# Performance work log

Measured on AMD Instinct MI355X. Metric: run time of the kernel, lower is better.

The kernel has to match this reference:

```python
import jax, jax.numpy as jnp
import numpy as np

D, H, T, P1, P2, B = 1024, 16, 2048, 16, 16, 2
HD = D // H
EPS = 1e-6
NEG = -1e30


def _ln(x, g, b):
    mu = jnp.mean(x, axis=-1, keepdims=True)
    var = jnp.mean((x - mu) ** 2, axis=-1, keepdims=True)
    return (x - mu) * jax.lax.rsqrt(var + EPS) * g + b


def _split_heads(x):  # [B,S,D] -> [B,H,S,HD]
    b, s, _ = x.shape
    return x.reshape(b, s, H, HD).transpose(0, 2, 1, 3)


def _merge_heads(x):  # [B,H,S,HD] -> [B,S,D]
    b, _, s, _ = x.shape
    return x.transpose(0, 2, 1, 3).reshape(b, s, D)


def setup_inputs() -> dict:
    key = jax.random.key(0)
    ks = jax.random.split(key, 24)
    s = 0.02
    inp = {
        'x': jax.random.normal(ks[0], (B, T, D), jnp.float32),
        'p1': jax.random.normal(ks[1], (B, P1, D), jnp.float32),
        'p2': jax.random.normal(ks[2], (B, P2, D), jnp.float32),
        'prior_1': jax.random.uniform(ks[3], (B, T), jnp.float32),
        'prior_2': jax.random.uniform(ks[4], (B, T), jnp.float32),
        'mask': jnp.ones((B, T), jnp.float32),
        'Wq': s * jax.random.normal(ks[5], (D, D), jnp.float32),
        'bq': jnp.zeros((D,), jnp.float32),
        'Wk': s * jax.random.normal(ks[6], (D, D), jnp.float32),
        'bk': jnp.zeros((D,), jnp.float32),
        'Wv': s * jax.random.normal(ks[7], (D, D), jnp.float32),
        'bv': jnp.zeros((D,), jnp.float32),
        'ln2_g': jnp.ones((D,), jnp.float32),
        'ln2_b': jnp.zeros((D,), jnp.float32),
        'W1': s * jax.random.normal(ks[8], (D, D), jnp.float32),
        'b1': jnp.zeros((D,), jnp.float32),
        'W2': s * jax.random.normal(ks[9], (D, D), jnp.float32),
        'b2': jnp.zeros((D,), jnp.float32),
        'Wp1': s * jax.random.normal(ks[10], (D, D), jnp.float32),
        'bp1': jnp.zeros((D,), jnp.float32),
        'Wp2': s * jax.random.normal(ks[11], (D, D), jnp.float32),
        'bp2': jnp.zeros((D,), jnp.float32),
    }
    return inp


def reference(x, p1, p2, prior_1, prior_2, mask, Wq, bq, Wk, bk, Wv, bv,
              ln2_g, ln2_b, W1, b1, W2, b2, Wp1, bp1, Wp2, bp2):
    scale = 1.0 / jnp.sqrt(jnp.asarray(HD, x.dtype))
    # Q/K are [proj(x); p1; p2] (prompts enter unprojected), V only from x.
    q = _split_heads(jnp.concatenate([x @ Wq + bq, p1, p2], axis=1))
    k = _split_heads(jnp.concatenate([x @ Wk + bk, p1, p2], axis=1))
    v = _split_heads(x @ Wv + bv)
    scores = jnp.einsum('bhqd,bhkd->bhqk', q, k) * scale  # [B,H,T+P,T+P]

    word = scores[:, :, :T, :T]                                  # [B,H,T,T]
    p1s = jnp.swapaxes(scores[:, :, :T, T:T + P1], -1, -2)       # [B,H,P1,T]
    p2s = jnp.swapaxes(scores[:, :, :T, T + P1:], -1, -2)        # [B,H,P2,T]

    word = word + (1.0 - mask)[:, None, None, :] * NEG           # mask_logits
    wa = jax.nn.softmax(word, axis=-1)
    p1a = jax.nn.softmax(jax.nn.softmax(p1s, axis=-1) * prior_1[:, None, None, :], axis=-1)
    p2a = jax.nn.softmax(jax.nn.softmax(p2s, axis=-1) * prior_2[:, None, None, :], axis=-1)

    ctx = jnp.einsum('bhqk,bhkd->bhqd', wa, v)    # [B,H,T,HD]
    p1_v = jnp.einsum('bhpk,bhkd->bhpd', p1a, ctx)
    p2_v = jnp.einsum('bhpk,bhkd->bhpd', p2a, ctx)

    residual = x + _merge_heads(ctx)
    out = _ln(residual, ln2_g, ln2_b)
    out = jax.nn.gelu(out @ W1 + b1, approximate=False)
    out = out @ W2 + b2 + residual

    p1_out = _ln(_merge_heads(p1_v) + p1, ln2_g, ln2_b)
    p1_out = jax.nn.gelu(p1_out @ Wp1 + bp1, approximate=False)

    p2_out = _ln(_merge_heads(p2_v) + p2, ln2_g, ln2_b)
    p2_out = jax.nn.gelu(p2_out @ Wp2 + bp2, approximate=False)
    return (out, p1_out, p2_out)
```

## Files before the change

kernel.cpp:

```cpp
#include <hip/hip_runtime.h>

#define DEV __device__ __forceinline__

typedef unsigned short u16;
typedef unsigned int   u32;
typedef short  s16x8  __attribute__((ext_vector_type(8)));
typedef float  f32x4  __attribute__((ext_vector_type(4)));
typedef float  f32x16 __attribute__((ext_vector_type(16)));

constexpr int Bc = 2, Hc = 16, Tc = 2048, Dc = 1024, HDc = 64, Mc = 4096;
constexpr int TP = Tc + 32;
constexpr float SCALEc = 0.125f;
constexpr float LOG2E = 1.44269504088896340736f;
constexpr float SCALE2c = SCALEc * LOG2E;
constexpr float NEGc = -1e30f;

typedef __attribute__((address_space(3))) void lds_void;
typedef const __attribute__((address_space(1))) void g_void;

DEV void gload16(const void* g, void* l) {
  __builtin_amdgcn_global_load_lds((g_void*)g, (lds_void*)l, 16, 0, 0);
}

DEV int swz(int r) { return (r & 7) ^ ((r >> 3) & 7); }

DEV u32 bfr(float f) {
  u32 u = __float_as_uint(f);
  return (u + 0x7fffu + ((u >> 16) & 1u)) >> 16;
}
DEV u32 cvtpk(float a, float b) {
  u32 r;
  asm("v_cvt_pk_bf16_f32 %0, %1, %2" : "=v"(r) : "v"(a), "v"(b));
  return r;
}
DEV s16x8 mk8(u32 w0, u32 w1, u32 w2, u32 w3) {
  union { u32 u[4]; s16x8 v; } x;
  x.u[0] = w0; x.u[1] = w1; x.u[2] = w2; x.u[3] = w3;
  return x.v;
}
DEV float geluf(float x) { return 0.5f * x * (1.0f + erff(x * 0.70710678118654752440f)); }

DEV float wredS(float v) {
  #pragma unroll
  for (int o = 32; o; o >>= 1) v += __shfl_xor(v, o);
  return v;
}
DEV float wredM(float v) {
  #pragma unroll
  for (int o = 32; o; o >>= 1) v = fmaxf(v, __shfl_xor(v, o));
  return v;
}
DEV float bredS(float v, float* sm) {
  v = wredS(v);
  __syncthreads();
  if ((threadIdx.x & 63) == 0) sm[threadIdx.x >> 6] = v;
  __syncthreads();
  return sm[0] + sm[1] + sm[2] + sm[3];
}
DEV float bredM(float v, float* sm) {
  v = wredM(v);
  __syncthreads();
  if ((threadIdx.x & 63) == 0) sm[threadIdx.x >> 6] = v;
  __syncthreads();
  return fmaxf(fmaxf(sm[0], sm[1]), fmaxf(sm[2], sm[3]));
}

__global__ __launch_bounds__(256) void transpose_w_k(const float* __restrict__ src,
                                                     u16* __restrict__ dst) {
  __shared__ float tile[32][33];
  int bx = blockIdx.x, by = blockIdx.y;
  int tx = threadIdx.x & 31, ty = threadIdx.x >> 5;
  #pragma unroll
  for (int i = 0; i < 32; i += 8)
    tile[ty + i][tx] = src[(size_t)(by * 32 + ty + i) * Dc + bx * 32 + tx];
  __syncthreads();
  #pragma unroll
  for (int i = 0; i < 32; i += 8)
    dst[(size_t)(bx * 32 + ty + i) * Dc + by * 32 + tx] = (u16)bfr(tile[tx][ty + i]);
}

__global__ __launch_bounds__(256) void cvt_bf16_k(const float* __restrict__ in,
                                                  u16* __restrict__ out, int n4) {
  int i = blockIdx.x * 256 + threadIdx.x;
  if (i < n4) {
    float4 v = ((const float4*)in)[i];
    ushort4 u;
    u.x = (u16)bfr(v.x); u.y = (u16)bfr(v.y); u.z = (u16)bfr(v.z); u.w = (u16)bfr(v.w);
    ((ushort4*)out)[i] = u;
  }
}

__global__ __launch_bounds__(256) void kprompt_k(const float* __restrict__ p1,
                                                 const float* __restrict__ p2,
                                                 u16* __restrict__ kb) {
  int i = blockIdx.x * 256 + threadIdx.x;
  int d = i & 63, j = (i >> 6) & 31, h = (i >> 11) & 15, b = i >> 15;
  float v = (j < 16) ? p1[(size_t)(b * 16 + j) * Dc + h * 64 + d]
                     : p2[(size_t)(b * 16 + j - 16) * Dc + h * 64 + d];
  kb[(((size_t)(b * Hc + h) * TP + Tc + j) << 6) + d] = (u16)bfr(v);
}

__global__ __launch_bounds__(256) void vtrans_k(const u16* __restrict__ vb,
                                                u16* __restrict__ vt) {
  __shared__ u16 tl[64][65];
  int bh = blockIdx.x >> 5, tc = blockIdx.x & 31;
  int d = threadIdx.x & 63, r = threadIdx.x >> 6;
  #pragma unroll
  for (int i = 0; i < 64; i += 4)
    tl[r + i][d] = vb[(((size_t)bh * Tc + tc * 64 + r + i) << 6) + d];
  __syncthreads();
  int t = threadIdx.x & 63, dd = threadIdx.x >> 6;
  #pragma unroll
  for (int i = 0; i < 64; i += 4)
    vt[((size_t)bh * 64 + dd + i) * Tc + tc * 64 + t] = tl[t][dd + i];
}

template <int MODE, int NBX>
__global__ __launch_bounds__(256, 3) void gemm128_k(
    const u16* __restrict__ A, const u16* __restrict__ Bt,
    const float* __restrict__ bias0, const float* __restrict__ bias1,
    const float* __restrict__ bias2,
    u16* __restrict__ outQ, u16* __restrict__ outK, u16* __restrict__ outV,
    u16* __restrict__ outB, float* __restrict__ outF,
    const float* __restrict__ resid) {
  __shared__ __align__(16) u16 smem[17408];
  u16* as0 = smem;
  u16* bs0 = smem + 2 * 128 * 32;
  const int tid = threadIdx.x, lane = tid & 63, wave = tid >> 6;
  const int wr = wave >> 1, wc = wave & 1;
  const int nwg = gridDim.x, bid = (int)blockIdx.x;
  const int wg = (bid & 7) * (nwg >> 3) + (bid >> 3);
  const int row0 = (wg % NBX) * 128, col0 = (wg / NBX) * 128;

  f32x4 zero4;
  #pragma unroll
  for (int r = 0; r < 4; ++r) zero4[r] = 0.f;
  f32x4 acc[4][4];
  #pragma unroll
  for (int i = 0; i < 4; ++i)
    #pragma unroll
    for (int j = 0; j < 4; ++j) acc[i][j] = zero4;

  auto stage = [&](int buf, int kt) {
    const int k0 = kt * 32;
    #pragma unroll
    for (int is = 0; is < 2; ++is) {
      int q = is * 256 + tid; int r = q >> 2, c = q & 3, g = c ^ ((r >> 1) & 3);
      gload16(A + (size_t)(row0 + r) * Dc + k0 + g * 8,
              as0 + (size_t)buf * 4096 + (is * 256 + wave * 64) * 8);
    }
    #pragma unroll
    for (int is = 0; is < 2; ++is) {
      int q = is * 256 + tid; int r = q >> 2, c = q & 3, g = c ^ ((r >> 1) & 3);
      gload16(Bt + (size_t)(col0 + r) * Dc + k0 + g * 8,
              bs0 + (size_t)buf * 4096 + (is * 256 + wave * 64) * 8);
    }
  };

  stage(0, 0);
  asm volatile("s_waitcnt vmcnt(0)" ::: "memory");
  __syncthreads();

  int cur = 0;
  for (int kt = 0; kt < 32; ++kt) {
    if (kt + 1 < 32) stage(cur ^ 1, kt + 1);
    s16x8 af[4], bfv[4];
    #pragma unroll
    for (int f = 0; f < 4; ++f) {
      int r = wr * 64 + f * 16 + (lane & 15);
      int c = (lane >> 4) ^ ((r >> 1) & 3);
      af[f] = *(const s16x8*)&as0[cur * 4096 + r * 32 + c * 8];
    }
    #pragma unroll
    for (int f = 0; f < 4; ++f) {
      int r = wc * 64 + f * 16 + (lane & 15);
      int c = (lane >> 4) ^ ((r >> 1) & 3);
      bfv[f] = *(const s16x8*)&bs0[cur * 4096 + r * 32 + c * 8];
    }
    __builtin_amdgcn_s_setprio(1);
    #pragma unroll
    for (int i = 0; i < 4; ++i)
      #pragma unroll
      for (int j = 0; j < 4; ++j)
        acc[i][j] = __builtin_amdgcn_mfma_f32_16x16x32_bf16(af[i], bfv[j], acc[i][j], 0, 0, 0);
    __builtin_amdgcn_s_setprio(0);
    __syncthreads();
    cur ^= 1;
  }

  if (MODE == 0 || MODE == 1) {
    const int CS = 136;
    u16* ct = smem;
    #pragma unroll
    for (int i = 0; i < 4; ++i)
      #pragma unroll
      for (int j = 0; j < 4; ++j)
        #pragma unroll
        for (int r = 0; r < 4; ++r) {
          int rl = wr * 64 + i * 16 + (lane >> 4) * 4 + r;
          int cl = wc * 64 + j * 16 + (lane & 15);
          float v = acc[i][j][r];
          if (MODE == 0) {
            int n = (col0 + cl) & 1023;
            int which = (col0 + cl) >> 10;
            v += (which == 0 ? bias0 : (which == 1 ? bias1 : bias2))[n];
          } else {
            v = geluf(v + bias0[col0 + cl]);
          }
          ct[rl * CS + cl] = (u16)bfr(v);
        }
    __syncthreads();
    #pragma unroll
    for (int it = 0; it < 16; ++it) {
      int linear = it * 256 + tid;
      int row = linear >> 5, c4 = (linear & 31) * 4;
      ushort4 val = *(const ushort4*)&ct[row * CS + c4];
      int grow = row0 + row;
      if (MODE == 1) {
        *(ushort4*)&outB[(size_t)grow * Dc + col0 + c4] = val;
      } else {
        int col = col0 + c4;
        int which = col >> 10, n = col & 1023;
        int hh = n >> 6, d = n & 63, bb = grow >> 11, t = grow & 2047;
        if (which == 0)
          *(ushort4*)&outQ[(((size_t)(bb * Hc + hh) * Tc + t) << 6) + d] = val;
        else if (which == 1)
          *(ushort4*)&outK[(((size_t)(bb * Hc + hh) * TP + t) << 6) + d] = val;
        else
          *(ushort4*)&outV[(((size_t)(bb * Hc + hh) * Tc + t) << 6) + d] = val;
      }
    }
  } else {
    const int CSF = 132;
    float* cf = (float*)smem;
    #pragma unroll
    for (int p = 0; p < 2; ++p) {
      if (wr == p) {
        #pragma unroll
        for (int i = 0; i < 4; ++i)
          #pragma unroll
          for (int j = 0; j < 4; ++j)
            #pragma unroll
            for (int r = 0; r < 4; ++r) {
              int rl = i * 16 + (lane >> 4) * 4 + r;
              int cl = wc * 64 + j * 16 + (lane & 15);
              cf[rl * CSF + cl] = acc[i][j][r];
            }
      }
      __syncthreads();
      #pragma unroll
      for (int it = 0; it < 8; ++it) {
        int linear = it * 256 + tid;
        int row = linear >> 5, c4 = (linear & 31) * 4;
        float4 v = *(const float4*)&cf[row * CSF + c4];
        int grow = row0 + p * 64 + row;
        int col = col0 + c4;
        float4 rr = *(const float4*)&resid[(size_t)grow * Dc + col];
        float4 o;
        o.x = v.x + bias0[col + 0] + rr.x;
        o.y = v.y + bias0[col + 1] + rr.y;
        o.z = v.z + bias0[col + 2] + rr.z;
        o.w = v.w + bias0[col + 3] + rr.w;
        *(float4*)&outF[(size_t)grow * Dc + col] = o;
      }
      __syncthreads();
    }
  }
}

__global__ __launch_bounds__(256, 2) void attn_k(
    const u16* __restrict__ qb,
    const u16* __restrict__ kb,
    const u16* __restrict__ vt,
    const float* __restrict__ maskp,
    float* __restrict__ OP0, float* __restrict__ OP1,
    float* __restrict__ ML) {
  __shared__ __align__(16) u16 kls[2][64 * 64];
  __shared__ __align__(16) u16 vls[2][64 * 64];
  __shared__ float mls[1024];

  const int tid = threadIdx.x, lane = tid & 63, wave = tid >> 6;
  const int wg = ((int)blockIdx.x & 7) * 128 + ((int)blockIdx.x >> 3);
  const int ks = wg & 1, qt = (wg >> 1) & 15, bh = wg >> 5;
  const int b = bh >> 4;
  const int lo = lane & 31, h5 = lane >> 5;
  const size_t kbase = (size_t)bh * TP * 64;
  const size_t vbase = (size_t)bh * 64 * Tc;

  for (int i = tid; i < 1024; i += 256)
    mls[i] = (1.0f - maskp[(size_t)b * Tc + ks * 1024 + i]) * NEGc;

  const int q0 = qt * 128 + wave * 32;
  s16x8 qf[4];
  #pragma unroll
  for (int kc = 0; kc < 4; ++kc)
    qf[kc] = *(const s16x8*)(qb + ((size_t)bh * Tc + q0 + lo) * 64 + kc * 16 + h5 * 8);

  auto stageKV = [&](int buf, int kt2) {
    #pragma unroll
    for (int is = 0; is < 2; ++is) {
      int q = is * 256 + tid; int r = q >> 3, c = q & 7, g = c ^ swz(r);
      gload16(kb + kbase + (size_t)(kt2 * 64 + r) * 64 + g * 8,
              &kls[buf][(is * 256 + wave * 64) * 8]);
      gload16(vt + vbase + (size_t)r * Tc + kt2 * 64 + g * 8,
              &vls[buf][(is * 256 + wave * 64) * 8]);
    }
  };

  stageKV(0, ks * 16);
  asm volatile("s_waitcnt vmcnt(0)" ::: "memory");
  __syncthreads();

  f32x16 zero16;
  #pragma unroll
  for (int r = 0; r < 16; ++r) zero16[r] = 0.f;
  f32x16 O0 = zero16, O1 = zero16, racc = zero16;

  int cur = 0;
  for (int kt = 0; kt < 16; ++kt) {
    if (kt + 1 < 16) stageKV(cur ^ 1, ks * 16 + kt + 1);

    #pragma unroll
    for (int c = 0; c < 2; ++c) {
      f32x16 s = zero16;
      __builtin_amdgcn_s_setprio(1);
      #pragma unroll
      for (int kc = 0; kc < 4; ++kc) {
        int r = c * 32 + lo;
        int ci = (kc * 2 + h5) ^ swz(r);
        s16x8 kf = *(const s16x8*)&kls[cur][r * 64 + ci * 8];
        s = __builtin_amdgcn_mfma_f32_32x32x16_bf16(kf, qf[kc], s, 0, 0, 0);
      }
      __builtin_amdgcn_s_setprio(0);

      float4 mq[4];
      #pragma unroll
      for (int g = 0; g < 4; ++g)
        mq[g] = *(const float4*)&mls[kt * 64 + c * 32 + 4 * h5 + 8 * g];

      float p[16];
      #pragma unroll
      for (int r = 0; r < 16; ++r) {
        float mv = (&mq[r >> 2].x)[r & 3];
        p[r] = exp2f(s[r] * SCALE2c + mv);
        racc[r] += p[r];
      }

      #pragma unroll
      for (int k1 = 0; k1 < 2; ++k1) {
        u32 w0 = cvtpk(p[8 * k1 + 0], p[8 * k1 + 1]);
        u32 w1 = cvtpk(p[8 * k1 + 2], p[8 * k1 + 3]);
        u32 w2 = cvtpk(p[8 * k1 + 4], p[8 * k1 + 5]);
        u32 w3 = cvtpk(p[8 * k1 + 6], p[8 * k1 + 7]);
        asm volatile("v_permlane32_swap_b32 %0, %1" : "+v"(w2), "+v"(w0));
        asm volatile("v_permlane32_swap_b32 %0, %1" : "+v"(w3), "+v"(w1));
        s16x8 pf = mk8(w0, w1, w2, w3);
        __builtin_amdgcn_s_setprio(1);
        #pragma unroll
        for (int db = 0; db < 2; ++db) {
          int d = db * 32 + lo;
          int ci = (c * 4 + k1 * 2 + h5) ^ swz(d);
          s16x8 vf = *(const s16x8*)&vls[cur][d * 64 + ci * 8];
          if (db == 0) O0 = __builtin_amdgcn_mfma_f32_32x32x16_bf16(pf, vf, O0, 0, 0, 0);
          else         O1 = __builtin_amdgcn_mfma_f32_32x32x16_bf16(pf, vf, O1, 0, 0, 0);
        }
        __builtin_amdgcn_s_setprio(0);
      }
    }
    __syncthreads();
    cur ^= 1;
  }

  float* dst = ks ? OP1 : OP0;
  #pragma unroll
  for (int r = 0; r < 16; ++r) {
    int row = q0 + (r & 3) + 8 * (r >> 2) + 4 * h5;
    dst[((size_t)bh * Tc + row) * 64 + lo]      = O0[r];
    dst[((size_t)bh * Tc + row) * 64 + 32 + lo] = O1[r];
  }
  float lt = 0.f;
  #pragma unroll
  for (int r = 0; r < 16; ++r) lt += racc[r];
  lt += __shfl_xor(lt, 32);
  if (lane < 32)
    ML[((size_t)ks * 32 + bh) * Tc + q0 + lo] = lt;
}

__global__ __launch_bounds__(256) void combine_k(const float* __restrict__ OP0,
                                                 const float* __restrict__ OP1,
                                                 const float* __restrict__ ML,
                                                 float* __restrict__ ctx) {
  int idx = blockIdx.x * 256 + threadIdx.x;
  int row = idx >> 4;
  int c4 = (idx & 15) * 4;
  float linv = 1.0f / (ML[(size_t)row] + ML[(size_t)32 * Tc + row]);
  float4 v0 = *(const float4*)(OP0 + (size_t)row * 64 + c4);
  float4 v1 = *(const float4*)(OP1 + (size_t)row * 64 + c4);
  float4 o;
  o.x = (v0.x + v1.x) * linv;
  o.y = (v0.y + v1.y) * linv;
  o.z = (v0.z + v1.z) * linv;
  o.w = (v0.w + v1.w) * linv;
  *(float4*)(ctx + (size_t)row * 64 + c4) = o;
}

__global__ __launch_bounds__(256) void promptsc_k(const u16* __restrict__ qb,
                                                  const u16* __restrict__ kb,
                                                  float* __restrict__ SP) {
  __shared__ __align__(16) u16 kpls[32 * 64];
  const int tid = threadIdx.x, lane = tid & 63, wave = tid >> 6;
  const int qt = blockIdx.x, bh = blockIdx.y;
  const int lo = lane & 31, h5 = lane >> 5;
  const size_t kbase = (size_t)bh * TP * 64;

  {
    int r = tid >> 3, c = tid & 7, g = c ^ swz(r);
    gload16(kb + kbase + (size_t)(Tc + r) * 64 + g * 8, &kpls[wave * 64 * 8]);
  }
  const int q0 = qt * 128 + wave * 32;
  s16x8 qf[4];
  #pragma unroll
  for (int kc = 0; kc < 4; ++kc)
    qf[kc] = *(const s16x8*)(qb + ((size_t)bh * Tc + q0 + lo) * 64 + kc * 16 + h5 * 8);
  asm volatile("s_waitcnt vmcnt(0)" ::: "memory");
  __syncthreads();

  f32x16 sp;
  #pragma unroll
  for (int r = 0; r < 16; ++r) sp[r] = 0.f;
  #pragma unroll
  for (int kc = 0; kc < 4; ++kc) {
    int ci = (kc * 2 + h5) ^ swz(lo);
    s16x8 kf = *(const s16x8*)&kpls[lo * 64 + ci * 8];
    sp = __builtin_amdgcn_mfma_f32_32x32x16_bf16(kf, qf[kc], sp, 0, 0, 0);
  }
  #pragma unroll
  for (int r = 0; r < 16; ++r) {
    int pr = (r & 3) + 8 * (r >> 2) + 4 * h5;
    SP[((size_t)bh * 32 + pr) * Tc + q0 + lo] = sp[r] * SCALEc;
  }
}

__global__ __launch_bounds__(256) void prompt_softmax_k(float* __restrict__ SP,
                                                        const float* __restrict__ pr1,
                                                        const float* __restrict__ pr2) {
  __shared__ float sm[4];
  int row = blockIdx.x;
  int bh = row >> 5, p = row & 31, b = bh >> 4;
  const float* prior = (p < 16 ? pr1 : pr2) + (size_t)b * Tc;
  float* s = SP + (size_t)row * Tc;
  int tid = threadIdx.x;
  float v[8], pw[8];
  #pragma unroll
  for (int i = 0; i < 8; ++i) { int t = tid + i * 256; v[i] = s[t]; pw[i] = prior[t]; }
  float mx = -INFINITY;
  #pragma unroll
  for (int i = 0; i < 8; ++i) mx = fmaxf(mx, v[i]);
  mx = bredM(mx, sm);
  float sum = 0.f;
  #pragma unroll
  for (int i = 0; i < 8; ++i) { v[i] = __expf(v[i] - mx); sum += v[i]; }
  sum = bredS(sum, sm);
  float inv = 1.0f / sum;
  float mx2 = -INFINITY;
  #pragma unroll
  for (int i = 0; i < 8; ++i) { v[i] = v[i] * inv * pw[i]; mx2 = fmaxf(mx2, v[i]); }
  mx2 = bredM(mx2, sm);
  float sum2 = 0.f;
  #pragma unroll
  for (int i = 0; i < 8; ++i) { v[i] = __expf(v[i] - mx2); sum2 += v[i]; }
  sum2 = bredS(sum2, sm);
  float inv2 = 1.0f / sum2;
  #pragma unroll
  for (int i = 0; i < 8; ++i) s[tid + i * 256] = v[i] * inv2;
}

__global__ __launch_bounds__(256) void pv_partial_k(const float* __restrict__ PA,
                                                    const float* __restrict__ ctx,
                                                    float* __restrict__ PVP) {
  __shared__ float pal[32][128];
  const int bh = blockIdx.x, ts = blockIdx.y;
  const int tid = threadIdx.x;
  const int t0 = ts * 128;
  const float* pabase = PA + (size_t)bh * 32 * Tc;

  #pragma unroll
  for (int i = 0; i < 4; ++i) {
    int e = tid + i * 256;
    int p = e >> 5, c4 = e & 31;
    *(float4*)&pal[p][c4 * 4] = *(const float4*)&pabase[(size_t)p * Tc + t0 + c4 * 4];
  }
  __syncthreads();

  const int d4 = tid & 15, p0 = tid >> 4;
  const float* cb = ctx + ((size_t)bh * Tc + t0) * 64 + d4 * 4;
  float4 a0 = make_float4(0.f, 0.f, 0.f, 0.f);
  float4 a1 = make_float4(0.f, 0.f, 0.f, 0.f);
  for (int tt = 0; tt < 128; ++tt) {
    float4 v = *(const float4*)(cb + (size_t)tt * 64);
    float w0 = pal[p0][tt], w1 = pal[p0 + 16][tt];
    a0.x += w0 * v.x; a0.y += w0 * v.y; a0.z += w0 * v.z; a0.w += w0 * v.w;
    a1.x += w1 * v.x; a1.y += w1 * v.y; a1.z += w1 * v.z; a1.w += w1 * v.w;
  }
  float* o = PVP + (((size_t)ts * 32 + bh) * 32) * 64 + d4 * 4;
  *(float4*)(o + (size_t)p0 * 64) = a0;
  *(float4*)(o + (size_t)(p0 + 16) * 64) = a1;
}

__global__ __launch_bounds__(256) void pv_reduce_k(const float* __restrict__ PVP,
                                                   float* __restrict__ PVo) {
  int e = blockIdx.x * 256 + threadIdx.x;
  float s = 0.f;
  #pragma unroll
  for (int ts = 0; ts < 16; ++ts) s += PVP[(size_t)ts * 65536 + e];
  PVo[e] = s;
}

__global__ __launch_bounds__(256) void resln_k(const float* __restrict__ x,
                                               const float* __restrict__ ctx,
                                               const float* __restrict__ g,
                                               const float* __restrict__ be,
                                               float* __restrict__ res,
                                               u16* __restrict__ lnout) {
  __shared__ float sm[4];
  int row = blockIdx.x;
  int b = row >> 11, t = row & 2047;
  int tid = threadIdx.x, c4 = tid * 4;
  int h = c4 >> 6, d = c4 & 63;
  float4 xv = *(const float4*)(x + (size_t)row * Dc + c4);
  float4 cv = *(const float4*)(ctx + (((size_t)(b * Hc + h) * Tc + t) << 6) + d);
  float r0 = xv.x + cv.x, r1 = xv.y + cv.y, r2 = xv.z + cv.z, r3 = xv.w + cv.w;
  float4 rr; rr.x = r0; rr.y = r1; rr.z = r2; rr.w = r3;
  *(float4*)(res + (size_t)row * Dc + c4) = rr;
  float s = bredS(r0 + r1 + r2 + r3, sm);
  float sq = bredS(r0 * r0 + r1 * r1 + r2 * r2 + r3 * r3, sm);
  float mu = s * (1.0f / Dc);
  float var = sq * (1.0f / Dc) - mu * mu;
  float rs = rsqrtf(var + 1e-6f);
  ushort4 o;
  o.x = (u16)bfr((r0 - mu) * rs * g[c4 + 0] + be[c4 + 0]);
  o.y = (u16)bfr((r1 - mu) * rs * g[c4 + 1] + be[c4 + 1]);
  o.z = (u16)bfr((r2 - mu) * rs * g[c4 + 2] + be[c4 + 2]);
  o.w = (u16)bfr((r3 - mu) * rs * g[c4 + 3] + be[c4 + 3]);
  *(ushort4*)(lnout + (size_t)row * Dc + c4) = o;
}

__global__ __launch_bounds__(256) void promptln_k(const float* __restrict__ PVo,
                                                  const float* __restrict__ p1,
                                                  const float* __restrict__ p2,
                                                  const float* __restrict__ g,
                                                  const float* __restrict__ be,
                                                  float* __restrict__ PMLN) {
  __shared__ float sm[4];
  int row = blockIdx.x;
  int b = row >> 5, j = row & 31;
  int tid = threadIdx.x, c4 = tid * 4;
  int h = c4 >> 6, d = c4 & 63;
  const float* pr = (j < 16) ? (p1 + (size_t)(b * 16 + j) * Dc + c4)
                             : (p2 + (size_t)(b * 16 + j - 16) * Dc + c4);
  float4 pv4 = *(const float4*)(PVo + (((size_t)(b * Hc + h) * 32 + j) << 6) + d);
  float4 pp4 = *(const float4*)pr;
  float r0 = pv4.x + pp4.x, r1 = pv4.y + pp4.y, r2 = pv4.z + pp4.z, r3 = pv4.w + pp4.w;
  float s = bredS(r0 + r1 + r2 + r3, sm);
  float sq = bredS(r0 * r0 + r1 * r1 + r2 * r2 + r3 * r3, sm);
  float mu = s * (1.0f / Dc);
  float var = sq * (1.0f / Dc) - mu * mu;
  float rs = rsqrtf(var + 1e-6f);
  float4 o;
  o.x = (r0 - mu) * rs * g[c4 + 0] + be[c4 + 0];
  o.y = (r1 - mu) * rs * g[c4 + 1] + be[c4 + 1];
  o.z = (r2 - mu) * rs * g[c4 + 2] + be[c4 + 2];
  o.w = (r3 - mu) * rs * g[c4 + 3] + be[c4 + 3];
  *(float4*)(PMLN + (size_t)row * Dc + c4) = o;
}

__global__ __launch_bounds__(256) void pffn_partial_k(const float* __restrict__ PMLN,
                                                      const float* __restrict__ Wp1,
                                                      const float* __restrict__ Wp2,
                                                      float* __restrict__ PB) {
  __shared__ float pm[32][32];
  const int tid = threadIdx.x;
  const int ks = blockIdx.x, ct = blockIdx.y, s = blockIdx.z;
  const int c = ct * 256 + tid;
  const int k0 = ks * 32;
  const float* W = s ? Wp2 : Wp1;

  #pragma unroll
  for (int i = 0; i < 4; ++i) {
    int e = tid + i * 256;
    int r = e >> 5, kk = e & 31;
    int grow = (r >> 4) * 32 + s * 16 + (r & 15);
    pm[r][kk] = PMLN[(size_t)grow * Dc + k0 + kk];
  }
  __syncthreads();

  float acc[32];
  #pragma unroll
  for (int r = 0; r < 32; ++r) acc[r] = 0.f;
  for (int kk = 0; kk < 32; ++kk) {
    float w = W[(size_t)(k0 + kk) * Dc + c];
    #pragma unroll
    for (int r = 0; r < 32; ++r) acc[r] += pm[r][kk] * w;
  }

  float* pb = PB + (((size_t)ks * 2 + s) * 32) * Dc + c;
  #pragma unroll
  for (int r = 0; r < 32; ++r) pb[(size_t)r * Dc] = acc[r];
}

__global__ __launch_bounds__(256) void pffn_reduce_k(const float* __restrict__ PB,
                                                     const float* __restrict__ bp1,
                                                     const float* __restrict__ bp2,
                                                     float* __restrict__ out) {
  int e = blockIdx.x * 256 + threadIdx.x;
  int s = e >> 15, rem = e & 32767;
  int r = rem >> 10, c = rem & 1023;
  float sum = 0.f;
  const float* pb = PB + ((size_t)s * 32 + r) * Dc + c;
  #pragma unroll
  for (int ks = 0; ks < 32; ++ks) sum += pb[(size_t)ks * 2 * 32 * Dc];
  const float* bp = s ? bp2 : bp1;
  out[(size_t)Mc * Dc + (size_t)s * (32 * Dc) + (size_t)r * Dc + c] = geluf(sum + bp[c]);
}

extern "C" void kernel_launch(void* const* d_in, const int* in_sizes, int n_in,
                              void* d_out, int out_size, void* d_ws, size_t ws_size,
                              hipStream_t stream) {
  (void)in_sizes; (void)n_in; (void)out_size; (void)ws_size;
  const float* x   = (const float*)d_in[0];
  const float* p1  = (const float*)d_in[1];
  const float* p2  = (const float*)d_in[2];
  const float* pr1 = (const float*)d_in[3];
  const float* pr2 = (const float*)d_in[4];
  const float* msk = (const float*)d_in[5];
  const float* Wq  = (const float*)d_in[6];
  const float* bq  = (const float*)d_in[7];
  const float* Wk  = (const float*)d_in[8];
  const float* bk  = (const float*)d_in[9];
  const float* Wv  = (const float*)d_in[10];
  const float* bv  = (const float*)d_in[11];
  const float* g2  = (const float*)d_in[12];
  const float* be2 = (const float*)d_in[13];
  const float* W1  = (const float*)d_in[14];
  const float* b1  = (const float*)d_in[15];
  const float* W2  = (const float*)d_in[16];
  const float* b2  = (const float*)d_in[17];
  const float* Wp1 = (const float*)d_in[18];
  const float* bp1 = (const float*)d_in[19];
  const float* Wp2 = (const float*)d_in[20];
  const float* bp2 = (const float*)d_in[21];

  char* ws = (char*)d_ws;
  size_t off = 0;
  auto alloc = [&](size_t bytes) {
    void* p = ws + off;
    off += (bytes + 255) & ~(size_t)255;
    return p;
  };
  u16* WQKVT = (u16*)alloc((size_t)3072 * 1024 * 2);
  u16* W1T   = (u16*)alloc((size_t)1024 * 1024 * 2);
  u16* W2T   = (u16*)alloc((size_t)1024 * 1024 * 2);
  u16* XB    = (u16*)alloc((size_t)Mc * Dc * 2);
  u16* QB    = (u16*)alloc((size_t)32 * Tc * 64 * 2);
  u16* KB    = (u16*)alloc((size_t)32 * TP * 64 * 2);
  u16* VB    = (u16*)alloc((size_t)32 * Tc * 64 * 2);
  u16* VT    = (u16*)alloc((size_t)32 * 64 * Tc * 2);
  float* CTX = (float*)alloc((size_t)32 * Tc * 64 * 4);
  float* SP  = (float*)alloc((size_t)32 * 32 * Tc * 4);
  float* PVo = (float*)alloc((size_t)32 * 32 * 64 * 4);
  float* RES = (float*)alloc((size_t)Mc * Dc * 4);
  float* PMLN = (float*)alloc((size_t)64 * Dc * 4);
  float* ML  = (float*)alloc((size_t)2 * 32 * Tc * 4);
  float* PVP = (float*)alloc((size_t)16 * 32 * 32 * 64 * 4);
  u16* LNOUT = XB;
  u16* H1    = VB;
  float* PB  = SP;
  float* OP0 = CTX;
  float* OP1 = RES;

  float* outMain = (float*)d_out;

  transpose_w_k<<<dim3(32, 32), 256, 0, stream>>>(Wq, WQKVT);
  transpose_w_k<<<dim3(32, 32), 256, 0, stream>>>(Wk, WQKVT + (size_t)1024 * 1024);
  transpose_w_k<<<dim3(32, 32), 256, 0, stream>>>(Wv, WQKVT + (size_t)2 * 1024 * 1024);
  transpose_w_k<<<dim3(32, 32), 256, 0, stream>>>(W1, W1T);
  transpose_w_k<<<dim3(32, 32), 256, 0, stream>>>(W2, W2T);
  cvt_bf16_k<<<4096, 256, 0, stream>>>(x, XB, (Mc * Dc) / 4);
  gemm128_k<0, 32><<<768, 256, 0, stream>>>(XB, WQKVT, bq, bk, bv, QB, KB, VB,
                                            nullptr, nullptr, nullptr);
  kprompt_k<<<256, 256, 0, stream>>>(p1, p2, KB);
  vtrans_k<<<1024, 256, 0, stream>>>(VB, VT);
  attn_k<<<1024, 256, 0, stream>>>(QB, KB, VT, msk, OP0, OP1, ML);
  promptsc_k<<<dim3(16, 32), 256, 0, stream>>>(QB, KB, SP);
  combine_k<<<4096, 256, 0, stream>>>(OP0, OP1, ML, CTX);
  prompt_softmax_k<<<1024, 256, 0, stream>>>(SP, pr1, pr2);
  pv_partial_k<<<dim3(32, 16), 256, 0, stream>>>(SP, CTX, PVP);
  pv_reduce_k<<<256, 256, 0, stream>>>(PVP, PVo);
  resln_k<<<4096, 256, 0, stream>>>(x, CTX, g2, be2, RES, LNOUT);
  promptln_k<<<64, 256, 0, stream>>>(PVo, p1, p2, g2, be2, PMLN);
  pffn_partial_k<<<dim3(32, 4, 2), 256, 0, stream>>>(PMLN, Wp1, Wp2, PB);
  pffn_reduce_k<<<256, 256, 0, stream>>>(PB, bp1, bp2, outMain);
  gemm128_k<1, 32><<<256, 256, 0, stream>>>(LNOUT, W1T, b1, nullptr, nullptr,
                                            nullptr, nullptr, nullptr, H1,
                                            nullptr, nullptr);
  gemm128_k<2, 32><<<256, 256, 0, stream>>>(H1, W2T, b2, nullptr, nullptr,
                                            nullptr, nullptr, nullptr, nullptr,
                                            outMain, RES);
}
```

Before: 236.6 us.

## Fuse split-K attention combine into attn kernel via in-block LDS reduction

Both key-split halves of a query tile now run in one 512-thread workgroup, each half with its own K/V LDS buffers. At the end the second half writes its partial output and row sums to LDS, and the first half normalizes and writes the context directly. This removes the separate combine kernel and the global round trip of two partial output buffers plus row sums. It doubles the LDS per block and adds an intra-block barrier and LDS exchange.

```diff
diff --git a/kernel.cpp b/kernel.cpp
--- a/kernel.cpp
+++ b/kernel.cpp
@@ -268,29 +268,31 @@
   }
 }
 
-__global__ __launch_bounds__(256, 2) void attn_k(
+__global__ __launch_bounds__(512, 2) void attn_k(
     const u16* __restrict__ qb,
     const u16* __restrict__ kb,
     const u16* __restrict__ vt,
     const float* __restrict__ maskp,
-    float* __restrict__ OP0, float* __restrict__ OP1,
-    float* __restrict__ ML) {
-  __shared__ __align__(16) u16 kls[2][64 * 64];
-  __shared__ __align__(16) u16 vls[2][64 * 64];
-  __shared__ float mls[1024];
+    float* __restrict__ ctx) {
+  __shared__ __align__(16) u16 kls[2][2][64 * 64];
+  __shared__ __align__(16) u16 vls[2][2][64 * 64];
+  __shared__ float mls[2048];
+  __shared__ float lse[128];
 
   const int tid = threadIdx.x, lane = tid & 63, wave = tid >> 6;
-  const int wg = ((int)blockIdx.x & 7) * 128 + ((int)blockIdx.x >> 3);
-  const int ks = wg & 1, qt = (wg >> 1) & 15, bh = wg >> 5;
+  const int ks = wave >> 2, w4 = wave & 3;
+  const int tl = tid & 255;
+  const int wg = ((int)blockIdx.x & 7) * 64 + ((int)blockIdx.x >> 3);
+  const int qt = wg & 15, bh = wg >> 4;
   const int b = bh >> 4;
   const int lo = lane & 31, h5 = lane >> 5;
   const size_t kbase = (size_t)bh * TP * 64;
   const size_t vbase = (size_t)bh * 64 * Tc;
 
-  for (int i = tid; i < 1024; i += 256)
-    mls[i] = (1.0f - maskp[(size_t)b * Tc + ks * 1024 + i]) * NEGc;
-
-  const int q0 = qt * 128 + wave * 32;
+  for (int i = tid; i < 2048; i += 512)
+    mls[i] = (1.0f - maskp[(size_t)b * Tc + i]) * NEGc;
+
+  const int q0 = qt * 128 + w4 * 32;
   s16x8 qf[4];
   #pragma unroll
   for (int kc = 0; kc < 4; ++kc)
@@ -299,11 +301,11 @@
   auto stageKV = [&](int buf, int kt2) {
     #pragma unroll
     for (int is = 0; is < 2; ++is) {
-      int q = is * 256 + tid; int r = q >> 3, c = q & 7, g = c ^ swz(r);
+      int q = is * 256 + tl; int r = q >> 3, c = q & 7, g = c ^ swz(r);
       gload16(kb + kbase + (size_t)(kt2 * 64 + r) * 64 + g * 8,
-              &kls[buf][(is * 256 + wave * 64) * 8]);
+              &kls[ks][buf][(is * 256 + w4 * 64) * 8]);
       gload16(vt + vbase + (size_t)r * Tc + kt2 * 64 + g * 8,
-              &vls[buf][(is * 256 + wave * 64) * 8]);
+              &vls[ks][buf][(is * 256 + w4 * 64) * 8]);
     }
   };
 
@@ -328,7 +330,7 @@
       for (int kc = 0; kc < 4; ++kc) {
         int r = c * 32 + lo;
         int ci = (kc * 2 + h5) ^ swz(r);
-        s16x8 kf = *(const s16x8*)&kls[cur][r * 64 + ci * 8];
+        s16x8 kf = *(const s16x8*)&kls[ks][cur][r * 64 + ci * 8];
         s = __builtin_amdgcn_mfma_f32_32x32x16_bf16(kf, qf[kc], s, 0, 0, 0);
       }
       __builtin_amdgcn_s_setprio(0);
@@ -336,7 +338,7 @@
       float4 mq[4];
       #pragma unroll
       for (int g = 0; g < 4; ++g)
-        mq[g] = *(const float4*)&mls[kt * 64 + c * 32 + 4 * h5 + 8 * g];
+        mq[g] = *(const float4*)&mls[ks * 1024 + kt * 64 + c * 32 + 4 * h5 + 8 * g];
 
       float p[16];
       #pragma unroll
@@ -360,7 +362,7 @@
         for (int db = 0; db < 2; ++db) {
           int d = db * 32 + lo;
           int ci = (c * 4 + k1 * 2 + h5) ^ swz(d);
-          s16x8 vf = *(const s16x8*)&vls[cur][d * 64 + ci * 8];
+          s16x8 vf = *(const s16x8*)&vls[ks][cur][d * 64 + ci * 8];
           if (db == 0) O0 = __builtin_amdgcn_mfma_f32_32x32x16_bf16(pf, vf, O0, 0, 0, 0);
           else         O1 = __builtin_amdgcn_mfma_f32_32x32x16_bf16(pf, vf, O1, 0, 0, 0);
         }
@@ -371,37 +373,37 @@
     cur ^= 1;
   }
 
-  float* dst = ks ? OP1 : OP0;
-  #pragma unroll
-  for (int r = 0; r < 16; ++r) {
-    int row = q0 + (r & 3) + 8 * (r >> 2) + 4 * h5;
-    dst[((size_t)bh * Tc + row) * 64 + lo]      = O0[r];
-    dst[((size_t)bh * Tc + row) * 64 + 32 + lo] = O1[r];
-  }
   float lt = 0.f;
   #pragma unroll
   for (int r = 0; r < 16; ++r) lt += racc[r];
   lt += __shfl_xor(lt, 32);
-  if (lane < 32)
-    ML[((size_t)ks * 32 + bh) * Tc + q0 + lo] = lt;
-}
-
-__global__ __launch_bounds__(256) void combine_k(const float* __restrict__ OP0,
-                                                 const float* __restrict__ OP1,
-                                                 const float* __restrict__ ML,
-                                                 float* __restrict__ ctx) {
-  int idx = blockIdx.x * 256 + threadIdx.x;
-  int row = idx >> 4;
-  int c4 = (idx & 15) * 4;
-  float linv = 1.0f / (ML[(size_t)row] + ML[(size_t)32 * Tc + row]);
-  float4 v0 = *(const float4*)(OP0 + (size_t)row * 64 + c4);
-  float4 v1 = *(const float4*)(OP1 + (size_t)row * 64 + c4);
-  float4 o;
-  o.x = (v0.x + v1.x) * linv;
-  o.y = (v0.y + v1.y) * linv;
-  o.z = (v0.z + v1.z) * linv;
-  o.w = (v0.w + v1.w) * linv;
-  *(float4*)(ctx + (size_t)row * 64 + c4) = o;
+
+  float* OexLo = (float*)kls[1];
+  float* OexHi = (float*)vls[1];
+  if (ks == 1) {
+    #pragma unroll
+    for (int r = 0; r < 16; ++r) {
+      int row = w4 * 32 + (r & 3) + 8 * (r >> 2) + 4 * h5;
+      OexLo[row * 32 + lo] = O0[r];
+      OexHi[row * 32 + lo] = O1[r];
+    }
+    if (lane < 32) lse[w4 * 32 + lo] = lt;
+  }
+  __syncthreads();
+  if (ks == 0) {
+    #pragma unroll
+    for (int r = 0; r < 16; ++r) {
+      int rq = (r & 3) + 8 * (r >> 2) + 4 * h5;
+      int row = w4 * 32 + rq;
+      float l0 = __shfl(lt, rq);
+      float linv = 1.0f / (l0 + lse[row]);
+      float o0 = O0[r] + OexLo[row * 32 + lo];
+      float o1 = O1[r] + OexHi[row * 32 + lo];
+      size_t base = ((size_t)bh * Tc + qt * 128 + row) * 64;
+      ctx[base + lo]      = o0 * linv;
+      ctx[base + 32 + lo] = o1 * linv;
+    }
+  }
 }
 
 __global__ __launch_bounds__(256) void promptsc_k(const u16* __restrict__ qb,
@@ -670,13 +672,10 @@
   float* PVo = (float*)alloc((size_t)32 * 32 * 64 * 4);
   float* RES = (float*)alloc((size_t)Mc * Dc * 4);
   float* PMLN = (float*)alloc((size_t)64 * Dc * 4);
-  float* ML  = (float*)alloc((size_t)2 * 32 * Tc * 4);
   float* PVP = (float*)alloc((size_t)16 * 32 * 32 * 64 * 4);
   u16* LNOUT = XB;
   u16* H1    = VB;
   float* PB  = SP;
-  float* OP0 = CTX;
-  float* OP1 = RES;
 
   float* outMain = (float*)d_out;
 
@@ -690,9 +689,8 @@
                                             nullptr, nullptr, nullptr);
   kprompt_k<<<256, 256, 0, stream>>>(p1, p2, KB);
   vtrans_k<<<1024, 256, 0, stream>>>(VB, VT);
-  attn_k<<<1024, 256, 0, stream>>>(QB, KB, VT, msk, OP0, OP1, ML);
+  attn_k<<<512, 512, 0, stream>>>(QB, KB, VT, msk, CTX);
   promptsc_k<<<dim3(16, 32), 256, 0, stream>>>(QB, KB, SP);
-  combine_k<<<4096, 256, 0, stream>>>(OP0, OP1, ML, CTX);
   prompt_softmax_k<<<1024, 256, 0, stream>>>(SP, pr1, pr2);
   pv_partial_k<<<dim3(32, 16), 256, 0, stream>>>(SP, CTX, PVP);
   pv_reduce_k<<<256, 256, 0, stream>>>(PVP, PVo);
```

New measurement: 241.4 us. 2.1% more time.
